# Kernel optimization log

Measured on AMD Instinct MI355X. Metric: run time of the kernel, lower is better.

Reference implementation:

```python
import jax, jax.numpy as jnp
import numpy as np


def setup_inputs() -> dict:
    key = jax.random.key(0)
    k1, k2, k3 = jax.random.split(key, 3)
    C, H, W = 64, 1024, 1024          # feature map from the UNet embed model
    N_PIX = H * W                      # every pixel belongs to one superpixel
    N_SEG = 4096                       # number of superpixels
    features = jax.random.normal(k1, (C, H, W), dtype=jnp.float32)
    pix_yx = jax.random.randint(k2, (N_PIX, 2), 0, H)          # (y, x) coords per pixel entry
    segment_ids = jax.random.randint(k3, (N_PIX,), 0, N_SEG)   # superpixel id per pixel entry
    return {"features": features, "pix_yx": pix_yx,
            "segment_ids": segment_ids, "n_segments": N_SEG}


def reference(features, pix_yx, segment_ids, n_segments):
    # features: [C, H, W]; pix_yx: [N, 2]; segment_ids: [N]
    # Equivalent to: for each superpixel i, mean of features[:, sp[:,-2], sp[:,-1]] over its pixels.
    gathered = features[:, pix_yx[:, 0], pix_yx[:, 1]].T          # [N, C] irregular gather
    sums = jax.ops.segment_sum(gathered, segment_ids,
                               num_segments=n_segments)           # [S, C]
    counts = jax.ops.segment_sum(jnp.ones_like(segment_ids, dtype=features.dtype),
                                 segment_ids, num_segments=n_segments)  # [S]
    # original asserts mass > 0; guard divide for any empty segment
    return sums / jnp.maximum(counts, 1.0)[:, None]               # [S, C]
```

## Files before the change

kernel.cpp:

```cpp
#include <hip/hip_runtime.h>
#include <stdint.h>

#define CCH 64
#define HW  (1024 * 1024)
#define NPIX (1024 * 1024)
#define NSEG 4096
#define NBIN 65536

typedef uint32_t u32x4 __attribute__((ext_vector_type(4)));

#define WS_NEED ((size_t)147456 * 1024)

__device__ inline uint32_t pack_bf16(float a, float b) {
    uint32_t ua = __float_as_uint(a), ub = __float_as_uint(b);
    ua = (ua + 0x7FFFu + ((ua >> 16) & 1u)) >> 16;
    ub = (ub + 0x7FFFu + ((ub >> 16) & 1u)) >> 16;
    return (ub << 16) | ua;
}
__device__ inline float bf_lo(uint32_t v) { return __uint_as_float(v << 16); }
__device__ inline float bf_hi(uint32_t v) { return __uint_as_float(v & 0xFFFF0000u); }

__global__ void k1_pack_hist(const int4* __restrict__ pix2,
                             const int2* __restrict__ seg2,
                             uint2* __restrict__ packed2,
                             uint32_t* __restrict__ poshist,
                             uint32_t* __restrict__ seghistPad) {
    int n = blockIdx.x * blockDim.x + threadIdx.x;
    int4 yx = pix2[n];
    int2 ss = seg2[n];
    uint32_t pos0 = ((uint32_t)yx.x << 10) | (uint32_t)yx.y;
    uint32_t pos1 = ((uint32_t)yx.z << 10) | (uint32_t)yx.w;
    packed2[n] = make_uint2(((uint32_t)ss.x << 20) | pos0,
                            ((uint32_t)ss.y << 20) | pos1);
    atomicAdd(&poshist[pos0 >> 4], 1u);
    atomicAdd(&poshist[pos1 >> 4], 1u);
    atomicAdd(&seghistPad[(uint32_t)ss.x * 16], 1u);
    atomicAdd(&seghistPad[(uint32_t)ss.y * 16], 1u);
}

__global__ void k2a_scan_local(const uint32_t* __restrict__ poshist,
                               uint32_t* __restrict__ posLocal,
                               uint32_t* __restrict__ posBlk) {
    __shared__ uint32_t sh[1024];
    int t = threadIdx.x, b = blockIdx.x;
    int i = b * 1024 + t;
    uint32_t v = poshist[i];
    sh[t] = v;
    __syncthreads();
    for (int off = 1; off < 1024; off <<= 1) {
        uint32_t u = (t >= off) ? sh[t - off] : 0u;
        __syncthreads();
        sh[t] += u;
        __syncthreads();
    }
    uint32_t inc = sh[t];
    posLocal[i] = inc - v;
    if (t == 1023) posBlk[b] = inc;
}

__global__ void k2b_scan_tops(const uint32_t* __restrict__ posBlk,
                              uint32_t* __restrict__ posBlkExc,
                              const uint32_t* __restrict__ seghistPad,
                              uint32_t* __restrict__ segOff,
                              uint32_t* __restrict__ segCursorPad) {
    int t = threadIdx.x;
    if (t < 64) {
        uint32_t v = posBlk[t];
        uint32_t x = v;
        for (int off = 1; off < 64; off <<= 1) {
            uint32_t u = __shfl_up(x, off);
            if ((t & 63) >= off) x += u;
        }
        posBlkExc[t] = x - v;
    }
    uint32_t c0 = seghistPad[(4 * t + 0) * 16];
    uint32_t c1 = seghistPad[(4 * t + 1) * 16];
    uint32_t c2 = seghistPad[(4 * t + 2) * 16];
    uint32_t c3 = seghistPad[(4 * t + 3) * 16];
    uint32_t tot = c0 + c1 + c2 + c3;
    __shared__ uint32_t sh[1024];
    sh[t] = tot;
    __syncthreads();
    for (int off = 1; off < 1024; off <<= 1) {
        uint32_t u = (t >= off) ? sh[t - off] : 0u;
        __syncthreads();
        sh[t] += u;
        __syncthreads();
    }
    uint32_t base = sh[t] - tot;
    uint32_t o0 = base, o1 = base + c0, o2 = o1 + c1, o3 = o2 + c2;
    ((uint4*)segOff)[t] = make_uint4(o0, o1, o2, o3);
    segCursorPad[(4 * t + 0) * 16] = o0;
    segCursorPad[(4 * t + 1) * 16] = o1;
    segCursorPad[(4 * t + 2) * 16] = o2;
    segCursorPad[(4 * t + 3) * 16] = o3;
}

__global__ void k2c_scan_add(const uint32_t* __restrict__ posLocal,
                             const uint32_t* __restrict__ posBlkExc,
                             uint32_t* __restrict__ posCursorPad) {
    int t = threadIdx.x, b = blockIdx.x;
    int i = b * 1024 + t;
    posCursorPad[(size_t)i * 16] = posLocal[i] + posBlkExc[b];
}

__global__ void k3_scatter(const uint2* __restrict__ packed2,
                           uint32_t* __restrict__ posCursorPad,
                           uint32_t* __restrict__ sorted) {
    int n = blockIdx.x * blockDim.x + threadIdx.x;
    uint2 p = packed2[n];
    uint32_t d0 = atomicAdd(&posCursorPad[(size_t)((p.x & 0xFFFFFu) >> 4) * 16], 1u);
    uint32_t d1 = atomicAdd(&posCursorPad[(size_t)((p.y & 0xFFFFFu) >> 4) * 16], 1u);
    sorted[d0] = p.x;
    sorted[d1] = p.y;
}

__global__ __launch_bounds__(256) void k4_gather(const float* __restrict__ feat,
                                                 const uint32_t* __restrict__ sorted,
                                                 uint32_t* __restrict__ segCursorPad,
                                                 uint32_t* __restrict__ gathered) {
    __shared__ uint32_t tile[256 * 36];
    __shared__ uint32_t rnk[256];
    const int tid = threadIdx.x;
    const int idx = blockIdx.x * 256 + tid;

    uint32_t pk = sorted[idx];
    const float* fp = feat + (pk & 0xFFFFFu);
    rnk[tid] = atomicAdd(&segCursorPad[(pk >> 20) * 16], 1u);

    float v[64];
#pragma unroll
    for (int c = 0; c < 64; ++c) {
        v[c] = fp[(size_t)c * HW];
    }
#pragma unroll
    for (int j = 0; j < 8; ++j) {
        u32x4 q = { pack_bf16(v[8 * j + 0], v[8 * j + 1]),
                    pack_bf16(v[8 * j + 2], v[8 * j + 3]),
                    pack_bf16(v[8 * j + 4], v[8 * j + 5]),
                    pack_bf16(v[8 * j + 6], v[8 * j + 7]) };
        *(u32x4*)&tile[tid * 36 + j * 4] = q;
    }
    __syncthreads();

    const int sub = tid & 7;
    const int rg  = tid >> 3;
#pragma unroll
    for (int it = 0; it < 8; ++it) {
        int row = it * 32 + rg;
        uint32_t r = rnk[row];
        u32x4 q = *(const u32x4*)&tile[row * 36 + sub * 4];
        __builtin_nontemporal_store(q, (u32x4*)(gathered + (size_t)r * 32 + sub * 4));
    }
}

__global__ __launch_bounds__(256) void k5_reduce(const uint32_t* __restrict__ gathered,
                                                 const uint32_t* __restrict__ segOff,
                                                 const uint32_t* __restrict__ seghistPad,
                                                 float* __restrict__ out) {
    const int s = blockIdx.x;
    const int tid = threadIdx.x;
    const int ch = tid & 7;
    const int rg = tid >> 3;
    uint32_t base = segOff[s];
    uint32_t cnt = seghistPad[s * 16];
    float acc[8] = {0.f, 0.f, 0.f, 0.f, 0.f, 0.f, 0.f, 0.f};
    const u32x4* g4 = (const u32x4*)gathered;
    for (uint32_t r = rg; r < cnt; r += 32) {
        u32x4 v = __builtin_nontemporal_load(&g4[(size_t)(base + r) * 8 + ch]);
        acc[0] += bf_lo(v.x); acc[1] += bf_hi(v.x);
        acc[2] += bf_lo(v.y); acc[3] += bf_hi(v.y);
        acc[4] += bf_lo(v.z); acc[5] += bf_hi(v.z);
        acc[6] += bf_lo(v.w); acc[7] += bf_hi(v.w);
    }
    __shared__ float red[256][8];
#pragma unroll
    for (int j = 0; j < 8; ++j) red[tid][j] = acc[j];
    __syncthreads();
    if (tid < 64) {
        int chunk = tid >> 3, j = tid & 7;
        float sum = 0.f;
#pragma unroll
        for (int g = 0; g < 32; ++g) sum += red[g * 8 + chunk][j];
        float inv = 1.0f / (float)(cnt ? cnt : 1u);
        out[s * 64 + tid] = sum * inv;
    }
}

__global__ __launch_bounds__(256) void k4_stream(const float* __restrict__ feat,
                                                 const uint32_t* __restrict__ sorted,
                                                 float* __restrict__ sums) {
    __shared__ float tile[64 * 65];
    __shared__ uint32_t epack[1024];
    const int tid = threadIdx.x;
    const int w = tid >> 6;
    const int l = tid & 63;
    const int base = blockIdx.x * 1024;
    for (int i = tid; i < 1024; i += 256) epack[i] = sorted[base + i];
    __syncthreads();
    for (int t = 0; t < 16; ++t) {
        uint32_t pk = epack[t * 64 + l];
        const float* fp = feat + (pk & 0xFFFFFu);
#pragma unroll
        for (int cc = 0; cc < 16; ++cc) {
            int c = (w << 4) + cc;
            tile[l * 65 + c] = fp[(size_t)c * HW];
        }
        __syncthreads();
#pragma unroll
        for (int pp = 0; pp < 16; ++pp) {
            int p = (w << 4) + pp;
            uint32_t sg = epack[t * 64 + p] >> 20;
            atomicAdd(&sums[sg * 64 + l], tile[p * 65 + l]);
        }
        __syncthreads();
    }
}

__global__ void k5_div(float* __restrict__ out, const uint32_t* __restrict__ seghistPad) {
    int i = blockIdx.x * blockDim.x + threadIdx.x;
    uint32_t cnt = seghistPad[(i >> 6) * 16];
    float c = (float)(cnt ? cnt : 1u);
    out[i] = out[i] / c;
}

extern "C" void kernel_launch(void* const* d_in, const int* in_sizes, int n_in,
                              void* d_out, int out_size, void* d_ws, size_t ws_size,
                              hipStream_t stream) {
    const float* feat = (const float*)d_in[0];
    const int*   pix  = (const int*)d_in[1];
    const int*   seg  = (const int*)d_in[2];
    float* out = (float*)d_out;

    uint8_t* ws = (uint8_t*)d_ws;
    uint32_t* packed       = (uint32_t*)(ws);
    uint32_t* sortedPos    = (uint32_t*)(ws + (size_t)4096 * 1024);
    uint32_t* poshist      = (uint32_t*)(ws + (size_t)8192 * 1024);
    uint32_t* seghistPad   = (uint32_t*)(ws + (size_t)8448 * 1024);
    uint32_t* posLocal     = (uint32_t*)(ws + (size_t)8704 * 1024);
    uint32_t* posBlk       = (uint32_t*)(ws + (size_t)8960 * 1024);
    uint32_t* posBlkExc    = (uint32_t*)(ws + (size_t)8964 * 1024);
    uint32_t* segOff       = (uint32_t*)(ws + (size_t)8968 * 1024);
    uint32_t* segCursorPad = (uint32_t*)(ws + (size_t)9216 * 1024);
    uint32_t* posCursorPad = (uint32_t*)(ws + (size_t)10240 * 1024);
    uint32_t* gathered     = (uint32_t*)(ws + (size_t)16384 * 1024);

    hipMemsetAsync(poshist, 0, (size_t)512 * 1024, stream);

    k1_pack_hist<<<NPIX / 512, 256, 0, stream>>>((const int4*)pix, (const int2*)seg,
                                                 (uint2*)packed, poshist, seghistPad);
    k2a_scan_local<<<64, 1024, 0, stream>>>(poshist, posLocal, posBlk);
    k2b_scan_tops<<<1, 1024, 0, stream>>>(posBlk, posBlkExc, seghistPad, segOff, segCursorPad);
    k2c_scan_add<<<64, 1024, 0, stream>>>(posLocal, posBlkExc, posCursorPad);
    k3_scatter<<<NPIX / 512, 256, 0, stream>>>((const uint2*)packed, posCursorPad, sortedPos);

    if (ws_size >= WS_NEED) {
        k4_gather<<<NPIX / 256, 256, 0, stream>>>(feat, sortedPos, segCursorPad, gathered);
        k5_reduce<<<NSEG, 256, 0, stream>>>(gathered, segOff, seghistPad, out);
    } else {
        hipMemsetAsync(out, 0, (size_t)NSEG * CCH * sizeof(float), stream);
        k4_stream<<<NPIX / 1024, 256, 0, stream>>>(feat, sortedPos, out);
        k5_div<<<(NSEG * CCH) / 256, 256, 0, stream>>>(out, seghistPad);
    }
}
```

Before: 603.5 us.

## Replace segment-sorted gather with channel-slab LDS atomic accumulation and partial reduction

Drops the second sort by segment (bf16 gathered buffer plus per-segment reduce). In its place, 256 blocks each own a 4-channel slab and a pixel range and accumulate per-segment sums in LDS with workgroup-scope float atomics, using an XOR swizzle to spread bank conflicts. A small kernel then reduces the 16 range partials and divides by the counts. The 64-entry block prefix is folded into scan_add, which removes the single-block top-scan kernel. This cuts the large intermediate write and read and the bf16 rounding, at the cost of LDS atomic contention and only 256 blocks of parallelism.

```diff
diff --git a/kernel.cpp b/kernel.cpp
--- a/kernel.cpp
+++ b/kernel.cpp
@@ -7,18 +7,12 @@
 #define NSEG 4096
 #define NBIN 65536
 
-typedef uint32_t u32x4 __attribute__((ext_vector_type(4)));
+#define SLABS 16
+#define CPS 4
+#define RANGES 16
+#define EPR (NPIX / RANGES)
 
-#define WS_NEED ((size_t)147456 * 1024)
-
-__device__ inline uint32_t pack_bf16(float a, float b) {
-    uint32_t ua = __float_as_uint(a), ub = __float_as_uint(b);
-    ua = (ua + 0x7FFFu + ((ua >> 16) & 1u)) >> 16;
-    ub = (ub + 0x7FFFu + ((ub >> 16) & 1u)) >> 16;
-    return (ub << 16) | ua;
-}
-__device__ inline float bf_lo(uint32_t v) { return __uint_as_float(v << 16); }
-__device__ inline float bf_hi(uint32_t v) { return __uint_as_float(v & 0xFFFF0000u); }
+#define WS_NEED ((size_t)29696 * 1024)
 
 __global__ void k1_pack_hist(const int4* __restrict__ pix2,
                              const int2* __restrict__ seg2,
@@ -58,50 +52,19 @@
     if (t == 1023) posBlk[b] = inc;
 }
 
-__global__ void k2b_scan_tops(const uint32_t* __restrict__ posBlk,
-                              uint32_t* __restrict__ posBlkExc,
-                              const uint32_t* __restrict__ seghistPad,
-                              uint32_t* __restrict__ segOff,
-                              uint32_t* __restrict__ segCursorPad) {
-    int t = threadIdx.x;
+__global__ void k2c_scan_add(const uint32_t* __restrict__ posLocal,
+                             const uint32_t* __restrict__ posBlk,
+                             uint32_t* __restrict__ posCursorPad) {
+    __shared__ uint32_t sbase;
+    int t = threadIdx.x, b = blockIdx.x;
     if (t < 64) {
-        uint32_t v = posBlk[t];
-        uint32_t x = v;
-        for (int off = 1; off < 64; off <<= 1) {
-            uint32_t u = __shfl_up(x, off);
-            if ((t & 63) >= off) x += u;
-        }
-        posBlkExc[t] = x - v;
+        uint32_t v = (t < b) ? posBlk[t] : 0u;
+        for (int off = 32; off; off >>= 1) v += __shfl_down(v, off);
+        if (t == 0) sbase = v;
     }
-    uint32_t c0 = seghistPad[(4 * t + 0) * 16];
-    uint32_t c1 = seghistPad[(4 * t + 1) * 16];
-    uint32_t c2 = seghistPad[(4 * t + 2) * 16];
-    uint32_t c3 = seghistPad[(4 * t + 3) * 16];
-    uint32_t tot = c0 + c1 + c2 + c3;
-    __shared__ uint32_t sh[1024];
-    sh[t] = tot;
     __syncthreads();
-    for (int off = 1; off < 1024; off <<= 1) {
-        uint32_t u = (t >= off) ? sh[t - off] : 0u;
-        __syncthreads();
-        sh[t] += u;
-        __syncthreads();
-    }
-    uint32_t base = sh[t] - tot;
-    uint32_t o0 = base, o1 = base + c0, o2 = o1 + c1, o3 = o2 + c2;
-    ((uint4*)segOff)[t] = make_uint4(o0, o1, o2, o3);
-    segCursorPad[(4 * t + 0) * 16] = o0;
-    segCursorPad[(4 * t + 1) * 16] = o1;
-    segCursorPad[(4 * t + 2) * 16] = o2;
-    segCursorPad[(4 * t + 3) * 16] = o3;
-}
-
-__global__ void k2c_scan_add(const uint32_t* __restrict__ posLocal,
-                             const uint32_t* __restrict__ posBlkExc,
-                             uint32_t* __restrict__ posCursorPad) {
-    int t = threadIdx.x, b = blockIdx.x;
     int i = b * 1024 + t;
-    posCursorPad[(size_t)i * 16] = posLocal[i] + posBlkExc[b];
+    posCursorPad[(size_t)i * 16] = posLocal[i] + sbase;
 }
 
 __global__ void k3_scatter(const uint2* __restrict__ packed2,
@@ -115,113 +78,57 @@
     sorted[d1] = p.y;
 }
 
-__global__ __launch_bounds__(256) void k4_gather(const float* __restrict__ feat,
+__global__ __launch_bounds__(1024) void k4_accum(const float* __restrict__ feat,
                                                  const uint32_t* __restrict__ sorted,
-                                                 uint32_t* __restrict__ segCursorPad,
-                                                 uint32_t* __restrict__ gathered) {
-    __shared__ uint32_t tile[256 * 36];
-    __shared__ uint32_t rnk[256];
+                                                 float* __restrict__ partials) {
+    __shared__ float sums[CPS * NSEG];
     const int tid = threadIdx.x;
-    const int idx = blockIdx.x * 256 + tid;
+    const int range = blockIdx.x >> 4;
+    const int slab  = blockIdx.x & 15;
+    for (int i = tid; i < CPS * NSEG; i += 1024) sums[i] = 0.f;
 
-    uint32_t pk = sorted[idx];
-    const float* fp = feat + (pk & 0xFFFFFu);
-    rnk[tid] = atomicAdd(&segCursorPad[(pk >> 20) * 16], 1u);
+    const uint2* sp = (const uint2*)(sorted + (size_t)range * EPR);
+    const float* fbase = feat + (size_t)(slab * CPS) * HW;
+    __syncthreads();
 
-    float v[64];
+    uint2 pk = sp[tid];
+    for (int it = 0; it < 32; ++it) {
+        uint2 cur = pk;
+        if (it < 31) pk = sp[(it + 1) * 1024 + tid];
+        uint32_t pos0 = cur.x & 0xFFFFFu, seg0 = cur.x >> 20;
+        uint32_t pos1 = cur.y & 0xFFFFFu, seg1 = cur.y >> 20;
 #pragma unroll
-    for (int c = 0; c < 64; ++c) {
-        v[c] = fp[(size_t)c * HW];
-    }
-#pragma unroll
-    for (int j = 0; j < 8; ++j) {
-        u32x4 q = { pack_bf16(v[8 * j + 0], v[8 * j + 1]),
-                    pack_bf16(v[8 * j + 2], v[8 * j + 3]),
-                    pack_bf16(v[8 * j + 4], v[8 * j + 5]),
-                    pack_bf16(v[8 * j + 6], v[8 * j + 7]) };
-        *(u32x4*)&tile[tid * 36 + j * 4] = q;
+        for (int j = 0; j < CPS; ++j) {
+            float v0 = __builtin_nontemporal_load(&fbase[(size_t)j * HW + pos0]);
+            float v1 = __builtin_nontemporal_load(&fbase[(size_t)j * HW + pos1]);
+            __hip_atomic_fetch_add(&sums[j * NSEG + (seg0 ^ (j << 2))], v0,
+                                   __ATOMIC_RELAXED, __HIP_MEMORY_SCOPE_WORKGROUP);
+            __hip_atomic_fetch_add(&sums[j * NSEG + (seg1 ^ (j << 2))], v1,
+                                   __ATOMIC_RELAXED, __HIP_MEMORY_SCOPE_WORKGROUP);
+        }
     }
     __syncthreads();
 
-    const int sub = tid & 7;
-    const int rg  = tid >> 3;
-#pragma unroll
-    for (int it = 0; it < 8; ++it) {
-        int row = it * 32 + rg;
-        uint32_t r = rnk[row];
-        u32x4 q = *(const u32x4*)&tile[row * 36 + sub * 4];
-        __builtin_nontemporal_store(q, (u32x4*)(gathered + (size_t)r * 32 + sub * 4));
+    float* pb = partials + ((size_t)(range * SLABS + slab)) * (CPS * NSEG);
+    for (int i = tid; i < CPS * NSEG; i += 1024) {
+        int j = i & 3, seg = i >> 2;
+        pb[i] = sums[j * NSEG + (seg ^ (j << 2))];
     }
 }
 
-__global__ __launch_bounds__(256) void k5_reduce(const uint32_t* __restrict__ gathered,
-                                                 const uint32_t* __restrict__ segOff,
-                                                 const uint32_t* __restrict__ seghistPad,
-                                                 float* __restrict__ out) {
-    const int s = blockIdx.x;
-    const int tid = threadIdx.x;
-    const int ch = tid & 7;
-    const int rg = tid >> 3;
-    uint32_t base = segOff[s];
-    uint32_t cnt = seghistPad[s * 16];
-    float acc[8] = {0.f, 0.f, 0.f, 0.f, 0.f, 0.f, 0.f, 0.f};
-    const u32x4* g4 = (const u32x4*)gathered;
-    for (uint32_t r = rg; r < cnt; r += 32) {
-        u32x4 v = __builtin_nontemporal_load(&g4[(size_t)(base + r) * 8 + ch]);
-        acc[0] += bf_lo(v.x); acc[1] += bf_hi(v.x);
-        acc[2] += bf_lo(v.y); acc[3] += bf_hi(v.y);
-        acc[4] += bf_lo(v.z); acc[5] += bf_hi(v.z);
-        acc[6] += bf_lo(v.w); acc[7] += bf_hi(v.w);
-    }
-    __shared__ float red[256][8];
+__global__ __launch_bounds__(256) void k5_red(const float* __restrict__ partials,
+                                              const uint32_t* __restrict__ seghistPad,
+                                              float* __restrict__ out) {
+    int g = blockIdx.x * 256 + threadIdx.x;
+    int slab = g >> 14;
+    int w = g & 16383;
+    float s = 0.f;
 #pragma unroll
-    for (int j = 0; j < 8; ++j) red[tid][j] = acc[j];
-    __syncthreads();
-    if (tid < 64) {
-        int chunk = tid >> 3, j = tid & 7;
-        float sum = 0.f;
-#pragma unroll
-        for (int g = 0; g < 32; ++g) sum += red[g * 8 + chunk][j];
-        float inv = 1.0f / (float)(cnt ? cnt : 1u);
-        out[s * 64 + tid] = sum * inv;
-    }
-}
-
-__global__ __launch_bounds__(256) void k4_stream(const float* __restrict__ feat,
-                                                 const uint32_t* __restrict__ sorted,
-                                                 float* __restrict__ sums) {
-    __shared__ float tile[64 * 65];
-    __shared__ uint32_t epack[1024];
-    const int tid = threadIdx.x;
-    const int w = tid >> 6;
-    const int l = tid & 63;
-    const int base = blockIdx.x * 1024;
-    for (int i = tid; i < 1024; i += 256) epack[i] = sorted[base + i];
-    __syncthreads();
-    for (int t = 0; t < 16; ++t) {
-        uint32_t pk = epack[t * 64 + l];
-        const float* fp = feat + (pk & 0xFFFFFu);
-#pragma unroll
-        for (int cc = 0; cc < 16; ++cc) {
-            int c = (w << 4) + cc;
-            tile[l * 65 + c] = fp[(size_t)c * HW];
-        }
-        __syncthreads();
-#pragma unroll
-        for (int pp = 0; pp < 16; ++pp) {
-            int p = (w << 4) + pp;
-            uint32_t sg = epack[t * 64 + p] >> 20;
-            atomicAdd(&sums[sg * 64 + l], tile[p * 65 + l]);
-        }
-        __syncthreads();
-    }
-}
-
-__global__ void k5_div(float* __restrict__ out, const uint32_t* __restrict__ seghistPad) {
-    int i = blockIdx.x * blockDim.x + threadIdx.x;
-    uint32_t cnt = seghistPad[(i >> 6) * 16];
-    float c = (float)(cnt ? cnt : 1u);
-    out[i] = out[i] / c;
+    for (int r = 0; r < RANGES; ++r)
+        s += partials[(((size_t)(r * SLABS + slab)) << 14) + w];
+    int seg = w >> 2, j = w & 3;
+    uint32_t cnt = seghistPad[seg * 16];
+    out[seg * 64 + slab * 4 + j] = s / (float)(cnt ? cnt : 1u);
 }
 
 extern "C" void kernel_launch(void* const* d_in, const int* in_sizes, int n_in,
@@ -239,27 +146,16 @@
     uint32_t* seghistPad   = (uint32_t*)(ws + (size_t)8448 * 1024);
     uint32_t* posLocal     = (uint32_t*)(ws + (size_t)8704 * 1024);
     uint32_t* posBlk       = (uint32_t*)(ws + (size_t)8960 * 1024);
-    uint32_t* posBlkExc    = (uint32_t*)(ws + (size_t)8964 * 1024);
-    uint32_t* segOff       = (uint32_t*)(ws + (size_t)8968 * 1024);
-    uint32_t* segCursorPad = (uint32_t*)(ws + (size_t)9216 * 1024);
-    uint32_t* posCursorPad = (uint32_t*)(ws + (size_t)10240 * 1024);
-    uint32_t* gathered     = (uint32_t*)(ws + (size_t)16384 * 1024);
+    uint32_t* posCursorPad = (uint32_t*)(ws + (size_t)9216 * 1024);
+    float*    partials     = (float*)   (ws + (size_t)13312 * 1024);
 
     hipMemsetAsync(poshist, 0, (size_t)512 * 1024, stream);
 
     k1_pack_hist<<<NPIX / 512, 256, 0, stream>>>((const int4*)pix, (const int2*)seg,
                                                  (uint2*)packed, poshist, seghistPad);
     k2a_scan_local<<<64, 1024, 0, stream>>>(poshist, posLocal, posBlk);
-    k2b_scan_tops<<<1, 1024, 0, stream>>>(posBlk, posBlkExc, seghistPad, segOff, segCursorPad);
-    k2c_scan_add<<<64, 1024, 0, stream>>>(posLocal, posBlkExc, posCursorPad);
+    k2c_scan_add<<<64, 1024, 0, stream>>>(posLocal, posBlk, posCursorPad);
     k3_scatter<<<NPIX / 512, 256, 0, stream>>>((const uint2*)packed, posCursorPad, sortedPos);
-
-    if (ws_size >= WS_NEED) {
-        k4_gather<<<NPIX / 256, 256, 0, stream>>>(feat, sortedPos, segCursorPad, gathered);
-        k5_reduce<<<NSEG, 256, 0, stream>>>(gathered, segOff, seghistPad, out);
-    } else {
-        hipMemsetAsync(out, 0, (size_t)NSEG * CCH * sizeof(float), stream);
-        k4_stream<<<NPIX / 1024, 256, 0, stream>>>(feat, sortedPos, out);
-        k5_div<<<(NSEG * CCH) / 256, 256, 0, stream>>>(out, seghistPad);
-    }
+    k4_accum<<<RANGES * SLABS, 1024, 0, stream>>>(feat, sortedPos, partials);
+    k5_red<<<(NSEG * CCH) / 256, 256, 0, stream>>>(partials, seghistPad, out);
 }
```

New measurement: 801.1 us. 1.33x slower.
